# Optimization experiments

Measured on AMD Instinct MI355X. Metric: run time of the kernel, lower is better.

## Reference

```python
import jax, jax.numpy as jnp
import numpy as np

B, S, D, H, I, OUT, L, M = 4, 896, 1024, 16, 4096, 4096, 2, 128
EPS = 1e-12

def _ln(x, g, b):
    mu = jnp.mean(x, -1, keepdims=True)
    var = jnp.mean((x - mu) ** 2, -1, keepdims=True)
    return (x - mu) * jax.lax.rsqrt(var + EPS) * g + b

def _attn(x, Wq, bq, Wk, bk, Wv, bv, Wo, bo, g, b):
    Bb, T, Dd = x.shape
    Dh = Dd // H
    q = (x @ Wq + bq).reshape(Bb, T, H, Dh).transpose(0, 2, 1, 3)
    k = (x @ Wk + bk).reshape(Bb, T, H, Dh).transpose(0, 2, 1, 3)
    v = (x @ Wv + bv).reshape(Bb, T, H, Dh).transpose(0, 2, 1, 3)
    scores = jnp.einsum('bhqd,bhkd->bhqk', q, k) / jnp.sqrt(jnp.float32(Dh)).astype(x.dtype)
    p = jax.nn.softmax(scores, axis=-1)
    o = jnp.einsum('bhqk,bhkd->bhqd', p, v).transpose(0, 2, 1, 3).reshape(Bb, T, Dd)
    return _ln(o @ Wo + bo + x, g, b)  # Residual: dense -> (dropout=0) -> LN(h + input)

def _ffn(x, Wm, bm, Wr, br, g, b):
    inter = jax.nn.gelu(x @ Wm + bm, approximate=False)
    return _ln(inter @ Wr + br + x, g, b)

def setup_inputs() -> dict:
    key = jax.random.key(0)
    ks = jax.random.split(key, 24)
    s = 0.02
    d = {
        'hidden_states': jax.random.normal(ks[0], (B, S, D), jnp.float32),
        'mem_emb': jnp.zeros((M, D), jnp.float32),  # read_memory_emb init zeros
        'Wq': jax.random.normal(ks[1], (L, D, D), jnp.float32) * s,
        'bq': jnp.zeros((L, D), jnp.float32),
        'Wk': jax.random.normal(ks[2], (L, D, D), jnp.float32) * s,
        'bk': jnp.zeros((L, D), jnp.float32),
        'Wv': jax.random.normal(ks[3], (L, D, D), jnp.float32) * s,
        'bv': jnp.zeros((L, D), jnp.float32),
        'Wo': jax.random.normal(ks[4], (L, D, D), jnp.float32) * s,
        'bo': jnp.zeros((L, D), jnp.float32),
        'ln1_g': jnp.ones((L, D), jnp.float32),
        'ln1_b': jnp.zeros((L, D), jnp.float32),
        'Wm': jax.random.normal(ks[5], (L, D, I), jnp.float32) * s,
        'bm': jnp.zeros((L, I), jnp.float32),
        'Wr': jax.random.normal(ks[6], (L, I, D), jnp.float32) * s,
        'br': jnp.zeros((L, D), jnp.float32),
        'ln2_g': jnp.ones((L, D), jnp.float32),
        'ln2_b': jnp.zeros((L, D), jnp.float32),
        'Wp': jax.random.normal(ks[7], (D, OUT), jnp.float32) * s,
        'bp': jnp.zeros((OUT,), jnp.float32),
    }
    return d

def reference(hidden_states, mem_emb, Wq, bq, Wk, bk, Wv, bv, Wo, bo, ln1_g, ln1_b,
              Wm, bm, Wr, br, ln2_g, ln2_b, Wp, bp):
    Bb = hidden_states.shape[0]
    read_mem = jnp.broadcast_to(mem_emb[None], (Bb, M, D))
    x = jnp.concatenate([read_mem, hidden_states], axis=1)  # pack [b, m+s, d]
    for l in range(L):
        x = _attn(x, Wq[l], bq[l], Wk[l], bk[l], Wv[l], bv[l], Wo[l], bo[l], ln1_g[l], ln1_b[l])
        x = _ffn(x, Wm[l], bm[l], Wr[l], br[l], ln2_g[l], ln2_b[l])
    read_out = x[:, :M]
    out = jax.nn.gelu(x[:, M:] @ Wp + bp, approximate=False)
    return (out, read_out)
```

## Files before the change

### kernel.cpp

```cpp
#include <hip/hip_runtime.h>
#include <math.h>

#define B_    4
#define S_    896
#define D_    1024
#define H_    16
#define I_    4096
#define OUT_  4096
#define L_    2
#define M_    128
#define T_    1024
#define NROW  4096
#define DH    64

typedef unsigned short u16;
typedef unsigned int   u32;
typedef float  f32x4  __attribute__((ext_vector_type(4)));
typedef float  f32x16 __attribute__((ext_vector_type(16)));
typedef __bf16 bf16x8 __attribute__((ext_vector_type(8)));
typedef u16    u16x2  __attribute__((ext_vector_type(2)));
typedef u16    u16x4  __attribute__((ext_vector_type(4)));

typedef __attribute__((address_space(1))) const void gvoid;
typedef __attribute__((address_space(3))) void       lvoid;

__device__ __forceinline__ u16 f2bf(float f) {
  u32 u = __builtin_bit_cast(u32, f);
  u = (u + 0x7fffu + ((u >> 16) & 1u)) >> 16;
  return (u16)u;
}
__device__ __forceinline__ float geluf(float v) {
  return 0.5f * v * (1.0f + erff(v * 0.70710678118654752f));
}
__device__ __forceinline__ void gld16(const void* g, void* l) {
  __builtin_amdgcn_global_load_lds((gvoid*)g, (lvoid*)l, 16, 0, 0);
}

__global__ __launch_bounds__(256) void build_x(const float* __restrict__ hs,
                                               const float* __restrict__ mem,
                                               float* __restrict__ xf,
                                               u16* __restrict__ xb) {
  const long i  = (long)blockIdx.x * 256 + threadIdx.x;
  const int row = (int)(i >> 8);
  const int c4  = (int)(i & 255);
  const int bb  = row >> 10, t = row & 1023;
  f32x4 v;
  if (t < M_) v = ((const f32x4*)(mem + (long)t * D_))[c4];
  else        v = ((const f32x4*)(hs + (long)(bb * S_ + (t - M_)) * D_))[c4];
  ((f32x4*)xf)[i] = v;
  u16x4 ob;
  #pragma unroll
  for (int c = 0; c < 4; c++) ob[c] = f2bf(v[c]);
  ((u16x4*)xb)[i] = ob;
}

__global__ __launch_bounds__(256) void wtrans(const float* __restrict__ W,
                                              u16* __restrict__ WT, int K, int N) {
  __shared__ float t[32][33];
  const int n0 = blockIdx.x * 32, k0 = blockIdx.y * 32;
  const int tx = threadIdx.x, ty = threadIdx.y;
  #pragma unroll
  for (int r = 0; r < 32; r += 8)
    t[ty + r][tx] = W[(long)(k0 + ty + r) * N + n0 + tx];
  __syncthreads();
  #pragma unroll
  for (int r = 0; r < 32; r += 8)
    WT[(long)(n0 + ty + r) * K + k0 + tx] = f2bf(t[tx][ty + r]);
}

__global__ __launch_bounds__(256) void lnred_k(const float* __restrict__ p0,
                                               const float* __restrict__ p1,
                                               const float* __restrict__ p2,
                                               const float* __restrict__ bias,
                                               const float* __restrict__ resid,
                                               const float* __restrict__ ga,
                                               const float* __restrict__ be,
                                               float* __restrict__ xf,
                                               u16* __restrict__ xb) {
  const int row = blockIdx.x, tid = threadIdx.x;
  const long ro = (long)row * D_;
  f32x4 v = ((const f32x4*)(p0 + ro))[tid];
  const f32x4 v1 = ((const f32x4*)(p1 + ro))[tid];
  const f32x4 v2 = ((const f32x4*)(p2 + ro))[tid];
  const f32x4 bi = ((const f32x4*)bias)[tid];
  const f32x4 rs4 = ((const f32x4*)(resid + ro))[tid];
  #pragma unroll
  for (int c = 0; c < 4; c++) v[c] = v[c] + v1[c] + v2[c] + bi[c] + rs4[c];
  float s  = v[0] + v[1] + v[2] + v[3];
  float ss = v[0]*v[0] + v[1]*v[1] + v[2]*v[2] + v[3]*v[3];
  #pragma unroll
  for (int m = 1; m < 64; m <<= 1) { s += __shfl_xor(s, m); ss += __shfl_xor(ss, m); }
  __shared__ float sm[8];
  if ((tid & 63) == 0) { sm[tid >> 6] = s; sm[4 + (tid >> 6)] = ss; }
  __syncthreads();
  s  = sm[0] + sm[1] + sm[2] + sm[3];
  ss = sm[4] + sm[5] + sm[6] + sm[7];
  const float mu  = s * (1.0f / D_);
  const float var = ss * (1.0f / D_) - mu * mu;
  const float rs  = rsqrtf(var + 1e-12f);
  const f32x4 gg = ((const f32x4*)ga)[tid];
  const f32x4 bb = ((const f32x4*)be)[tid];
  f32x4 o; u16x4 ob;
  #pragma unroll
  for (int c = 0; c < 4; c++) { o[c] = (v[c] - mu) * rs * gg[c] + bb[c]; ob[c] = f2bf(o[c]); }
  ((f32x4*)(xf + ro))[tid] = o;
  ((u16x4*)(xb + ro))[tid] = ob;
}

__global__ __launch_bounds__(256) void copy_ro(const float* __restrict__ xf,
                                               float* __restrict__ dst) {
  const long i  = (long)blockIdx.x * 256 + threadIdx.x;
  const int row = (int)(i >> 8);
  const int c4  = (int)(i & 255);
  const int bb  = row >> 7, t = row & 127;
  f32x4 v = ((const f32x4*)(xf + (long)(bb * T_ + t) * D_))[c4];
  ((f32x4*)dst)[i] = v;
}

template <int EPI, int RMAP>
__global__ __launch_bounds__(256) void gemm_bt(const u16* __restrict__ A,
                                               const u16* __restrict__ BT,
                                               const float* __restrict__ bias0,
                                               const float* __restrict__ bias1,
                                               const float* __restrict__ bias2,
                                               float* __restrict__ of,
                                               u16* __restrict__ ob0,
                                               u16* __restrict__ ob1,
                                               u16* __restrict__ ob2,
                                               int M, int N, int K, int KC) {
  __shared__ u16 As[128 * 32];
  __shared__ u16 Bs[128 * 32];
  const int tid = threadIdx.x;
  const int l   = tid & 63;
  const int w   = tid >> 6;
  const int r16 = l & 15;
  const int g   = l >> 4;
  const int bm = blockIdx.x, bn = blockIdx.y;

  const int kstart = (EPI == 4) ? blockIdx.z * KC : 0;
  const int klen   = (EPI == 4) ? min(KC, K - kstart) : K;

  const int srow0 = w * 16 + (l >> 2);
  const int srow1 = srow0 + 64;
  const int scol  = (l & 3) * 8;
  long ar0 = (long)bm * 128 + srow0;
  long ar1 = (long)bm * 128 + srow1;
  if (RMAP == 1) {
    int R0 = (int)ar0, R1 = (int)ar1;
    ar0 = (long)(R0 / 896) * 1024 + 128 + (R0 % 896);
    ar1 = (long)(R1 / 896) * 1024 + 128 + (R1 % 896);
  }
  const u16* Ag0 = A + ar0 * K + kstart + scol;
  const u16* Ag1 = A + ar1 * K + kstart + scol;
  const u16* Bg0 = BT + ((long)bn * 128 + srow0) * K + kstart + scol;
  const u16* Bg1 = BT + ((long)bn * 128 + srow1) * K + kstart + scol;
  u16* AsD0 = As + w * 512; u16* AsD1 = As + (w + 4) * 512;
  u16* BsD0 = Bs + w * 512; u16* BsD1 = Bs + (w + 4) * 512;

  const int wm = w >> 1, wn = w & 1;
  const int aro = (wm * 64 + r16) * 32 + g * 8;
  const int bro = (wn * 64 + r16) * 32 + g * 8;

  f32x4 acc[4][4];
  #pragma unroll
  for (int i = 0; i < 4; i++)
    #pragma unroll
    for (int j = 0; j < 4; j++) acc[i][j] = (f32x4){0.f, 0.f, 0.f, 0.f};

  for (int k0 = 0; k0 < klen; k0 += 32) {
    gld16(Ag0 + k0, AsD0);
    gld16(Ag1 + k0, AsD1);
    gld16(Bg0 + k0, BsD0);
    gld16(Bg1 + k0, BsD1);
    __syncthreads();
    bf16x8 af[4], bfr[4];
    #pragma unroll
    for (int i = 0; i < 4; i++) af[i]  = *(const bf16x8*)&As[aro + i * 512];
    #pragma unroll
    for (int j = 0; j < 4; j++) bfr[j] = *(const bf16x8*)&Bs[bro + j * 512];
    #pragma unroll
    for (int i = 0; i < 4; i++)
      #pragma unroll
      for (int j = 0; j < 4; j++)
        acc[i][j] = __builtin_amdgcn_mfma_f32_16x16x32_bf16(af[i], bfr[j], acc[i][j], 0, 0, 0);
    __syncthreads();
  }

  float* pof = (EPI == 4) ? of + (long)blockIdx.z * ((long)M * N) : of;
  #pragma unroll
  for (int i = 0; i < 4; i++) {
    const int grow0 = bm * 128 + wm * 64 + i * 16 + g * 4;
    #pragma unroll
    for (int j = 0; j < 4; j++) {
      const int gcol = bn * 128 + wn * 64 + j * 16 + r16;
      f32x4 v = acc[i][j];
      if (EPI == 0) {
        const int bb = grow0 >> 10, t0 = grow0 & 1023;
        if (gcol < 1024) {
          const float bi = bias0[gcol];
          const int h = gcol >> 6, d = gcol & 63;
          u16* dst = ob0 + ((long)(bb * H_ + h) * T_) * DH + d;
          #pragma unroll
          for (int rr = 0; rr < 4; rr++) dst[(long)(t0 + rr) * DH] = f2bf((v[rr] + bi) * 0.125f);
        } else if (gcol < 2048) {
          const int c = gcol - 1024;
          const float bi = bias1[c];
          const int h = c >> 6, d = c & 63;
          u16* dst = ob1 + ((long)(bb * H_ + h) * T_) * DH + d;
          #pragma unroll
          for (int rr = 0; rr < 4; rr++) dst[(long)(t0 + rr) * DH] = f2bf(v[rr] + bi);
        } else {
          const int c = gcol - 2048;
          const float bi = bias2[c];
          const int h = c >> 6, d = c & 63;
          u16x4 pk;
          #pragma unroll
          for (int rr = 0; rr < 4; rr++) pk[rr] = f2bf(v[rr] + bi);
          *(u16x4*)(ob2 + ((long)(bb * H_ + h) * DH + d) * T_ + t0) = pk;
        }
      } else if (EPI == 2) {
        const float bi = bias0[gcol];
        #pragma unroll
        for (int rr = 0; rr < 4; rr++)
          ob0[(long)(grow0 + rr) * N + gcol] = f2bf(geluf(v[rr] + bi));
      } else if (EPI == 3) {
        const float bi = bias0[gcol];
        #pragma unroll
        for (int rr = 0; rr < 4; rr++)
          of[(long)(grow0 + rr) * N + gcol] = geluf(v[rr] + bi);
      } else {
        #pragma unroll
        for (int rr = 0; rr < 4; rr++)
          pof[(long)(grow0 + rr) * N + gcol] = v[rr];
      }
    }
  }
}

__global__ __launch_bounds__(256) void attn_k(const u16* __restrict__ qB,
                                              const u16* __restrict__ kB,
                                              const u16* __restrict__ vT,
                                              u16* __restrict__ ctx) {
  const int l   = threadIdx.x & 63, w = threadIdx.x >> 6;
  const int q31 = l & 31, hl = l >> 5;
  const int bh  = blockIdx.y, bb = bh >> 4, h = bh & 15;
  const int qbase = (blockIdx.x * 4 + w) * 32;
  const u16* qh = qB + (long)bh * T_ * DH;
  const u16* kh = kB + (long)bh * T_ * DH;
  const u16* vh = vT + (long)bh * DH * T_;

  bf16x8 qf[4];
  #pragma unroll
  for (int d0 = 0; d0 < 4; d0++)
    qf[d0] = *(const bf16x8*)&qh[(qbase + q31) * DH + d0 * 16 + hl * 8];

  f32x16 ot0, ot1;
  #pragma unroll
  for (int i = 0; i < 16; i++) { ot0[i] = 0.f; ot1[i] = 0.f; }
  float m = -1e30f, lsum = 0.f;

  for (int kb0 = 0; kb0 < T_; kb0 += 32) {
    bf16x8 vf0a = *(const bf16x8*)&vh[q31 * T_ + kb0 + hl * 8];
    bf16x8 vf0b = *(const bf16x8*)&vh[q31 * T_ + kb0 + 16 + hl * 8];
    bf16x8 vf1a = *(const bf16x8*)&vh[(32 + q31) * T_ + kb0 + hl * 8];
    bf16x8 vf1b = *(const bf16x8*)&vh[(32 + q31) * T_ + kb0 + 16 + hl * 8];

    f32x16 st;
    #pragma unroll
    for (int i = 0; i < 16; i++) st[i] = 0.f;
    #pragma unroll
    for (int d0 = 0; d0 < 4; d0++) {
      bf16x8 kf = *(const bf16x8*)&kh[(kb0 + q31) * DH + d0 * 16 + hl * 8];
      st = __builtin_amdgcn_mfma_f32_32x32x16_bf16(kf, qf[d0], st, 0, 0, 0);
    }

    float x0 = fmaxf(st[0], st[1]),   x1 = fmaxf(st[2], st[3]);
    float x2 = fmaxf(st[4], st[5]),   x3 = fmaxf(st[6], st[7]);
    float x4 = fmaxf(st[8], st[9]),   x5 = fmaxf(st[10], st[11]);
    float x6 = fmaxf(st[12], st[13]), x7 = fmaxf(st[14], st[15]);
    float pm = fmaxf(fmaxf(fmaxf(x0, x1), fmaxf(x2, x3)),
                     fmaxf(fmaxf(x4, x5), fmaxf(x6, x7)));
    {
      float a = pm, b = pm;
      asm("v_permlane32_swap_b32 %0, %1" : "+v"(a), "+v"(b));
      pm = fmaxf(a, b);
    }

    if (!__all(pm <= m + 8.0f)) {
      const float nm = fmaxf(m, pm);
      const float sc = __expf(m - nm);
      m = nm;
      lsum *= sc;
      #pragma unroll
      for (int i = 0; i < 16; i++) { ot0[i] *= sc; ot1[i] *= sc; }
    }

    float p[16], sum = 0.f;
    #pragma unroll
    for (int i = 0; i < 16; i++) { p[i] = __expf(st[i] - m); sum += p[i]; }
    {
      float a = sum, b = sum;
      asm("v_permlane32_swap_b32 %0, %1" : "+v"(a), "+v"(b));
      sum = a + b;
    }
    lsum += sum;

    u32 pk[8];
    #pragma unroll
    for (int i = 0; i < 8; i++)
      asm("v_cvt_pk_bf16_f32 %0, %1, %2" : "=v"(pk[i]) : "v"(p[2 * i]), "v"(p[2 * i + 1]));
    asm("v_permlane32_swap_b32 %0, %1" : "+v"(pk[0]), "+v"(pk[2]));
    asm("v_permlane32_swap_b32 %0, %1" : "+v"(pk[1]), "+v"(pk[3]));
    asm("v_permlane32_swap_b32 %0, %1" : "+v"(pk[4]), "+v"(pk[6]));
    asm("v_permlane32_swap_b32 %0, %1" : "+v"(pk[5]), "+v"(pk[7]));
    union { u32 u[4]; bf16x8 v; } f1, f2;
    f1.u[0] = pk[0]; f1.u[1] = pk[1]; f1.u[2] = pk[2]; f1.u[3] = pk[3];
    f2.u[0] = pk[4]; f2.u[1] = pk[5]; f2.u[2] = pk[6]; f2.u[3] = pk[7];

    ot0 = __builtin_amdgcn_mfma_f32_32x32x16_bf16(vf0a, f1.v, ot0, 0, 0, 0);
    ot0 = __builtin_amdgcn_mfma_f32_32x32x16_bf16(vf0b, f2.v, ot0, 0, 0, 0);
    ot1 = __builtin_amdgcn_mfma_f32_32x32x16_bf16(vf1a, f1.v, ot1, 0, 0, 0);
    ot1 = __builtin_amdgcn_mfma_f32_32x32x16_bf16(vf1b, f2.v, ot1, 0, 0, 0);
  }

  const float inv = 1.0f / lsum;
  u16* dst = ctx + ((long)(bb * T_ + qbase + q31)) * D_ + h * DH;
  #pragma unroll
  for (int rg = 0; rg < 4; rg++) {
    u16x4 o0, o1;
    #pragma unroll
    for (int r = 0; r < 4; r++) {
      o0[r] = f2bf(ot0[rg * 4 + r] * inv);
      o1[r] = f2bf(ot1[rg * 4 + r] * inv);
    }
    const int d0 = rg * 8 + hl * 4;
    *(u16x4*)(dst + d0) = o0;
    *(u16x4*)(dst + 32 + d0) = o1;
  }
}

extern "C" void kernel_launch(void* const* d_in, const int* in_sizes, int n_in,
                              void* d_out, int out_size, void* d_ws, size_t ws_size,
                              hipStream_t stream) {
  const float* hs  = (const float*)d_in[0];
  const float* mem = (const float*)d_in[1];
  const float* Wq  = (const float*)d_in[2];
  const float* bq  = (const float*)d_in[3];
  const float* Wk  = (const float*)d_in[4];
  const float* bk  = (const float*)d_in[5];
  const float* Wv  = (const float*)d_in[6];
  const float* bv  = (const float*)d_in[7];
  const float* Wo  = (const float*)d_in[8];
  const float* bo  = (const float*)d_in[9];
  const float* g1  = (const float*)d_in[10];
  const float* be1 = (const float*)d_in[11];
  const float* Wm  = (const float*)d_in[12];
  const float* bm  = (const float*)d_in[13];
  const float* Wr  = (const float*)d_in[14];
  const float* br  = (const float*)d_in[15];
  const float* g2  = (const float*)d_in[16];
  const float* be2 = (const float*)d_in[17];
  const float* Wp  = (const float*)d_in[18];
  const float* bp  = (const float*)d_in[19];
  float* out = (float*)d_out;

  char* ws = (char*)d_ws;
  float* xf  = (float*)(ws + 0);
  u16*   xb  = (u16*)  (ws + 16777216);
  float* p0  = (float*)(ws + 25165824);
  float* p1  = (float*)(ws + 41943040);
  float* p2  = (float*)(ws + 58720256);
  u16*   qb  = (u16*)  (ws + 75497472);
  u16*   kb2 = (u16*)  (ws + 83886080);
  u16*   vtb = (u16*)  (ws + 92274688);
  u16*   ctx = (u16*)  (ws + 100663296);
  u16*   ib  = qb;
  u16*   WTqkv = (u16*)(ws + 109051904);
  u16*   WTo   = (u16*)(ws + 115343360);
  u16*   WTm   = (u16*)(ws + 117440512);
  u16*   WTr   = (u16*)(ws + 125829120);
  u16*   WTp   = WTqkv;

  const dim3 blk(256);
  const dim3 tb(32, 8);

  build_x<<<dim3(4096), blk, 0, stream>>>(hs, mem, xf, xb);

  for (int l = 0; l < L_; l++) {
    wtrans<<<dim3(32, 32), tb, 0, stream>>>(Wq + (long)l * D_ * D_, WTqkv, 1024, 1024);
    wtrans<<<dim3(32, 32), tb, 0, stream>>>(Wk + (long)l * D_ * D_, WTqkv + 1024 * 1024, 1024, 1024);
    wtrans<<<dim3(32, 32), tb, 0, stream>>>(Wv + (long)l * D_ * D_, WTqkv + 2048 * 1024, 1024, 1024);
    wtrans<<<dim3(32, 32), tb, 0, stream>>>(Wo + (long)l * D_ * D_, WTo, 1024, 1024);
    wtrans<<<dim3(128, 32), tb, 0, stream>>>(Wm + (long)l * D_ * I_, WTm, 1024, 4096);
    wtrans<<<dim3(32, 128), tb, 0, stream>>>(Wr + (long)l * I_ * D_, WTr, 4096, 1024);

    gemm_bt<0, 0><<<dim3(32, 24), blk, 0, stream>>>(xb, WTqkv,
        bq + l * D_, bk + l * D_, bv + l * D_,
        nullptr, qb, kb2, vtb, NROW, 3072, 1024, 0);
    attn_k<<<dim3(8, 64), blk, 0, stream>>>(qb, kb2, vtb, ctx);
    gemm_bt<4, 0><<<dim3(32, 8, 3), blk, 0, stream>>>(ctx, WTo,
        nullptr, nullptr, nullptr,
        p0, nullptr, nullptr, nullptr, NROW, 1024, 1024, 352);
    lnred_k<<<dim3(4096), blk, 0, stream>>>(p0, p1, p2, bo + l * D_, xf,
        g1 + l * D_, be1 + l * D_, xf, xb);
    gemm_bt<2, 0><<<dim3(32, 32), blk, 0, stream>>>(xb, WTm,
        bm + l * I_, nullptr, nullptr,
        nullptr, ib, nullptr, nullptr, NROW, 4096, 1024, 0);
    gemm_bt<4, 0><<<dim3(32, 8, 3), blk, 0, stream>>>(ib, WTr,
        nullptr, nullptr, nullptr,
        p0, nullptr, nullptr, nullptr, NROW, 1024, 4096, 1376);
    lnred_k<<<dim3(4096), blk, 0, stream>>>(p0, p1, p2, br + l * D_, xf,
        g2 + l * D_, be2 + l * D_, xf, xb);
  }

  wtrans<<<dim3(128, 32), tb, 0, stream>>>(Wp, WTp, 1024, 4096);
  gemm_bt<3, 1><<<dim3(28, 32), blk, 0, stream>>>(xb, WTp,
      bp, nullptr, nullptr,
      out, nullptr, nullptr, nullptr, 3584, 4096, 1024, 0);
  copy_ro<<<dim3(512), blk, 0, stream>>>(xf, out + 14680064);
}
```

Measured before the change: 844.6 us.

## Double-buffer LDS tiles in bf16 GEMM to overlap global loads with MFMA

The GEMM kernel now uses two LDS buffers for the A and B tiles. It issues the direct-to-LDS loads for the next K tile before running the MFMAs on the current tile, and keeps a single barrier per iteration. This is meant to hide global-load latency behind compute instead of stalling on a barrier right after each load. LDS use per block doubles, which may reduce occupancy. Correctness depends on the wait that covers the async loads before the trailing __syncthreads.

```diff
diff --git a/kernel.cpp b/kernel.cpp
--- a/kernel.cpp
+++ b/kernel.cpp
@@ -128,8 +128,8 @@
                                                u16* __restrict__ ob1,
                                                u16* __restrict__ ob2,
                                                int M, int N, int K, int KC) {
-  __shared__ u16 As[128 * 32];
-  __shared__ u16 Bs[128 * 32];
+  __shared__ u16 As[2 * 128 * 32];
+  __shared__ u16 Bs[2 * 128 * 32];
   const int tid = threadIdx.x;
   const int l   = tid & 63;
   const int w   = tid >> 6;
@@ -154,8 +154,7 @@
   const u16* Ag1 = A + ar1 * K + kstart + scol;
   const u16* Bg0 = BT + ((long)bn * 128 + srow0) * K + kstart + scol;
   const u16* Bg1 = BT + ((long)bn * 128 + srow1) * K + kstart + scol;
-  u16* AsD0 = As + w * 512; u16* AsD1 = As + (w + 4) * 512;
-  u16* BsD0 = Bs + w * 512; u16* BsD1 = Bs + (w + 4) * 512;
+  const int sd0 = w * 512, sd1 = (w + 4) * 512;
 
   const int wm = w >> 1, wn = w & 1;
   const int aro = (wm * 64 + r16) * 32 + g * 8;
@@ -167,23 +166,37 @@
     #pragma unroll
     for (int j = 0; j < 4; j++) acc[i][j] = (f32x4){0.f, 0.f, 0.f, 0.f};
 
-  for (int k0 = 0; k0 < klen; k0 += 32) {
-    gld16(Ag0 + k0, AsD0);
-    gld16(Ag1 + k0, AsD1);
-    gld16(Bg0 + k0, BsD0);
-    gld16(Bg1 + k0, BsD1);
-    __syncthreads();
+  const int nt = klen >> 5;
+  gld16(Ag0, As + sd0);
+  gld16(Ag1, As + sd1);
+  gld16(Bg0, Bs + sd0);
+  gld16(Bg1, Bs + sd1);
+  __syncthreads();
+
+  int cur = 0;
+  for (int kt = 0; kt < nt; ++kt) {
+    const int nxt = cur ^ 1;
+    if (kt + 1 < nt) {
+      const int ko = (kt + 1) << 5;
+      gld16(Ag0 + ko, As + nxt * 4096 + sd0);
+      gld16(Ag1 + ko, As + nxt * 4096 + sd1);
+      gld16(Bg0 + ko, Bs + nxt * 4096 + sd0);
+      gld16(Bg1 + ko, Bs + nxt * 4096 + sd1);
+    }
+    const u16* Asr = As + cur * 4096;
+    const u16* Bsr = Bs + cur * 4096;
     bf16x8 af[4], bfr[4];
     #pragma unroll
-    for (int i = 0; i < 4; i++) af[i]  = *(const bf16x8*)&As[aro + i * 512];
-    #pragma unroll
-    for (int j = 0; j < 4; j++) bfr[j] = *(const bf16x8*)&Bs[bro + j * 512];
+    for (int i = 0; i < 4; i++) af[i]  = *(const bf16x8*)&Asr[aro + i * 512];
+    #pragma unroll
+    for (int j = 0; j < 4; j++) bfr[j] = *(const bf16x8*)&Bsr[bro + j * 512];
     #pragma unroll
     for (int i = 0; i < 4; i++)
       #pragma unroll
       for (int j = 0; j < 4; j++)
         acc[i][j] = __builtin_amdgcn_mfma_f32_16x16x32_bf16(af[i], bfr[j], acc[i][j], 0, 0, 0);
     __syncthreads();
+    cur = nxt;
   }
 
   float* pof = (EPI == 4) ? of + (long)blockIdx.z * ((long)M * N) : of;
```

After: 809.8 us. -4.1%, faster.
